# Kernel tuning notes

Measured on AMD Instinct MI355X. Metric: run time of the kernel, lower is better.

Reference implementation:

```python
import jax, jax.numpy as jnp
import numpy as np
from jax import lax

B, CIN, COUT, H, W, K = 8, 256, 256, 64, 64, 3
KK = K * K
PAD, STRIDE = 1, 1
EPS = 1e-5


def setup_inputs() -> dict:
    key = jax.random.key(0)
    k0, k1, k2 = jax.random.split(key, 3)
    x = jax.random.normal(k0, (B, CIN, H, W), jnp.float32)
    # offset/mask predicting conv: 3*K*K output channels (o1, o2, mask)
    w_off = jax.random.normal(k1, (3 * KK, CIN, K, K), jnp.float32) * 0.01
    b_off = jnp.zeros((3 * KK,), jnp.float32)
    # main deformable conv weight
    weight = jax.random.normal(k2, (COUT, CIN, K, K), jnp.float32) / np.sqrt(CIN * KK).astype(np.float32)
    bias = jnp.zeros((COUT,), jnp.float32)
    gamma = jnp.ones((COUT,), jnp.float32)
    beta = jnp.zeros((COUT,), jnp.float32)
    return {"x": x, "w_off": w_off, "b_off": b_off, "weight": weight,
            "bias": bias, "gamma": gamma, "beta": beta}


def _bilinear_sample(img, ph, pw):
    """img: [C,H,W]; ph,pw: [KK,H,W] float sample positions. Zero outside. -> [C,KK,H,W]"""
    h0 = jnp.floor(ph).astype(jnp.int32)
    w0 = jnp.floor(pw).astype(jnp.int32)
    h1, w1 = h0 + 1, w0 + 1
    lh = ph - h0.astype(ph.dtype)
    lw = pw - w0.astype(pw.dtype)
    hh, hw = 1.0 - lh, 1.0 - lw

    def corner(hi, wi):
        valid = (hi >= 0) & (hi < H) & (wi >= 0) & (wi < W)
        hc = jnp.clip(hi, 0, H - 1)
        wc = jnp.clip(wi, 0, W - 1)
        v = img[:, hc, wc]  # [C,KK,H,W]
        return v * valid.astype(img.dtype)[None]

    return (corner(h0, w0) * (hh * hw)[None] + corner(h0, w1) * (hh * lw)[None]
            + corner(h1, w0) * (lh * hw)[None] + corner(h1, w1) * (lh * lw)[None])


def _forward(x, w_off, b_off, weight, bias, gamma, beta):
    dn = ('NCHW', 'OIHW', 'NCHW')
    # offset/mask branch (standard conv)
    om = lax.conv_general_dilated(x, w_off, (STRIDE, STRIDE), ((PAD, PAD), (PAD, PAD)),
                                  dimension_numbers=dn) + b_off[None, :, None, None]
    o1, o2, m = jnp.split(om, 3, axis=1)
    offset = jnp.concatenate([o1, o2], axis=1)          # [B, 2*KK, H, W]
    off_h = offset[:, 0::2]                             # [B, KK, H, W] dy per tap
    off_w = offset[:, 1::2]                             # [B, KK, H, W] dx per tap
    mask = jax.nn.sigmoid(m)                            # [B, KK, H, W]

    taps = jnp.arange(KK)
    base_h = (taps // K - PAD).astype(jnp.float32)[:, None, None] \
        + (jnp.arange(H, dtype=jnp.float32) * STRIDE)[None, :, None]  # [KK,H,1]
    base_w = (taps % K - PAD).astype(jnp.float32)[:, None, None] \
        + (jnp.arange(W, dtype=jnp.float32) * STRIDE)[None, None, :]  # [KK,1,W]
    ph = base_h[None] + off_h                           # [B,KK,H,W]
    pw = base_w[None] + off_w

    sampled = jax.vmap(_bilinear_sample)(x, ph, pw)     # [B,CIN,KK,H,W]
    sampled = sampled * mask[:, None]                   # modulated (DCNv2)

    y = jnp.einsum('bckhw,ock->bohw', sampled, weight.reshape(COUT, CIN, KK))
    y = y + bias[None, :, None, None]

    # BatchNorm2d (training mode: batch statistics) + ReLU
    mean = y.mean(axis=(0, 2, 3))
    var = y.var(axis=(0, 2, 3))
    yn = (y - mean[None, :, None, None]) * lax.rsqrt(var + EPS)[None, :, None, None]
    out = jax.nn.relu(gamma[None, :, None, None] * yn + beta[None, :, None, None])
    return out


def reference(x, w_off, b_off, weight, bias, gamma, beta):
    return _forward(x, w_off, b_off, weight, bias, gamma, beta)
```

## Files before the change

kernel.cpp:

```cpp
#include <hip/hip_runtime.h>
#include <cstdint>

#define BB    8
#define CIN   256
#define COUT  256
#define HH    64
#define WW    64

typedef __attribute__((ext_vector_type(8))) short    s16x8;
typedef __attribute__((ext_vector_type(8))) unsigned short u16x8;
typedef __attribute__((ext_vector_type(4))) unsigned short u16x4;
typedef __attribute__((ext_vector_type(4))) float    f32x4;

__device__ __forceinline__ float bf2f(unsigned short u) {
    unsigned int v = ((unsigned int)u) << 16;
    return __builtin_bit_cast(float, v);
}
__device__ __forceinline__ unsigned short f2bf(float f) {
    unsigned int u = __builtin_bit_cast(unsigned int, f);
    unsigned int r = (u + 0x7FFFu + ((u >> 16) & 1u)) >> 16;
    return (unsigned short)r;
}

__global__ void k_pack(const float* __restrict__ x,
                       const float* __restrict__ w,
                       const float* __restrict__ woff,
                       unsigned short* __restrict__ xT,
                       unsigned short* __restrict__ wTk,
                       unsigned short* __restrict__ wofT) {
    int blk = blockIdx.x;
    int t = threadIdx.x;
    __shared__ float tile[64 * 65];
    if (blk < 2048) {
        int b    = blk & 7;
        int rest = blk >> 3;
        int h    = rest >> 2;
        int c0   = (rest & 3) * 64;
#pragma unroll
        for (int r = 0; r < 16; ++r) {
            int idx = t + r * 256;
            int i = idx >> 6, w_ = idx & 63;
            tile[i * 65 + w_] = x[(((b * 256 + c0 + i) * 64 + h) * 64) + w_];
        }
        __syncthreads();
#pragma unroll
        for (int r = 0; r < 2; ++r) {
            int idx = t + r * 256;
            int w_ = idx >> 3;
            int c8 = (idx & 7) * 8;
            u16x8 res;
#pragma unroll
            for (int k = 0; k < 8; ++k) res[k] = f2bf(tile[(c8 + k) * 65 + w_]);
            *reinterpret_cast<u16x8*>(&xT[((b * 64 + h) * 64 + w_) * 256 + c0 + c8]) = res;
        }
    } else if (blk < 4352) {
        int idx = (blk - 2048) * 256 + t;
        int j   = idx & 7;
        int q   = (idx >> 3) & 3;
        int o16 = (idx >> 5) & 15;
        int n16 = (idx >> 9) & 15;
        int kc  = (idx >> 13) & 7;
        int tp  = idx >> 16;
        int c = kc * 32 + q * 8 + j;
        int o = n16 * 16 + o16;
        wTk[idx] = f2bf(w[(o * 256 + c) * 9 + tp]);
    } else {
        int idx = (blk - 4352) * 256 + t;
        int c  = idx & 255;
        int j  = (idx >> 8) & 31;
        int tp = idx >> 13;
        wofT[idx] = f2bf((j < 27) ? woff[(j * 256 + c) * 9 + tp] : 0.f);
    }
}

__global__ __launch_bounds__(512, 4)
void k_main(const unsigned short* __restrict__ xT,
            const unsigned short* __restrict__ wTk,
            const unsigned short* __restrict__ wofT,
            const float* __restrict__ boffg,
            const float* __restrict__ bias,
            unsigned short* __restrict__ y16,
            float* __restrict__ gsum, float* __restrict__ gssq) {
    __shared__ __align__(16) char smem[76032];
    int blk = blockIdx.x;
    int b = blk & 7, h = blk >> 3;
    int pblk = b * 64 + h;
    int t = threadIdx.x;
    int lane = t & 63, wv = t >> 6;
    int lm = lane & 15, q = lane >> 4;
    const f32x4 FZ = {0.f, 0.f, 0.f, 0.f};

    {
        unsigned short* S3 = (unsigned short*)smem;
        float* OMS = (float*)(smem + 67584);
        f32x4 oacc0 = FZ, oacc1 = FZ;
        int p0w = wv * 16;
        for (int cc = 0; cc < 2; ++cc) {
            __syncthreads();
            if (t < 96) {
                int rr = t >> 5, col = (t >> 4) & 1, c8 = (t & 15) * 8;
                u16x8 z = {0,0,0,0,0,0,0,0};
                *reinterpret_cast<u16x8*>(&S3[(rr * 66 + col * 65) * 136 + c8]) = z;
            }
#pragma unroll
            for (int r = 0; r < 6; ++r) {
                int v = t + r * 512;
                int rr = v >> 10, rem = v & 1023;
                int w_ = rem >> 4, c8 = (rem & 15) * 8;
                int hr = h + rr - 1;
                u16x8 d = {0,0,0,0,0,0,0,0};
                if (hr >= 0 && hr < 64)
                    d = *reinterpret_cast<const u16x8*>(xT + ((b * 64 + hr) * 64 + w_) * 256 + cc * 128 + c8);
                *reinterpret_cast<u16x8*>(&S3[(rr * 66 + w_ + 1) * 136 + c8]) = d;
            }
            __syncthreads();
            if (wv < 4) {
#pragma unroll
                for (int tp = 0; tp < 9; ++tp) {
                    int dh = tp / 3, dw = tp % 3;
                    const unsigned short* wb = wofT + (tp * 32 + lm) * 256 + cc * 128;
#pragma unroll
                    for (int kc = 0; kc < 4; ++kc) {
                        s16x8 a = *reinterpret_cast<const s16x8*>(
                            &S3[(dh * 66 + p0w + lm + dw) * 136 + kc * 32 + q * 8]);
                        s16x8 b0 = *reinterpret_cast<const s16x8*>(wb + kc * 32 + q * 8);
                        s16x8 b1 = *reinterpret_cast<const s16x8*>(wb + 16 * 256 + kc * 32 + q * 8);
                        oacc0 = __builtin_amdgcn_mfma_f32_16x16x32_bf16(a, b0, oacc0, 0, 0, 0);
                        oacc1 = __builtin_amdgcn_mfma_f32_16x16x32_bf16(a, b1, oacc1, 0, 0, 0);
                    }
                }
            }
        }
        if (wv < 4) {
#pragma unroll
            for (int n = 0; n < 2; ++n) {
                int j = n * 16 + lm;
                float bj = (j < 27) ? boffg[j] : 0.f;
                f32x4 a = n ? oacc1 : oacc0;
#pragma unroll
                for (int i = 0; i < 4; ++i)
                    OMS[(p0w + q * 4 + i) * 33 + j] = a[i] + bj;
            }
        }
        __syncthreads();
    }

    unsigned short* S = (unsigned short*)smem;
    float* OMS = (float*)(smem + 67584);
    f32x4 acc[4][4];
#pragma unroll
    for (int m = 0; m < 4; ++m)
#pragma unroll
        for (int n = 0; n < 4; ++n) acc[m][n] = FZ;

    if (wv >= 4) {
        int pw = wv - 4;
        int s  = lane & 7;
        int pA = pw * 16 + (lane >> 3);
        int pB = pA + 8;
        int rb = b * 4096;

        float wgA[4], wgB[4];
        int   adA[4], adB[4];

        auto setup = [&](int tp, int p, float* wgt, int* ad) {
            float oh = OMS[p * 33 + 2 * tp];
            float ow = OMS[p * 33 + 2 * tp + 1];
            float mv = OMS[p * 33 + 18 + tp];
            float mk = 1.f / (1.f + __expf(-mv));
            float ph = (float)(h + tp / 3 - 1) + oh;
            float pw_ = (float)(p + tp % 3 - 1) + ow;
            float fh0 = floorf(ph), fw0 = floorf(pw_);
            int ih0 = (int)fh0, iw0 = (int)fw0;
            float lh = ph - fh0, lw = pw_ - fw0;
            float hh = 1.f - lh, hw_ = 1.f - lw;
            bool vh0 = (ih0 >= 0) & (ih0 < 64);
            bool vh1 = (ih0 + 1 >= 0) & (ih0 + 1 < 64);
            bool vw0 = (iw0 >= 0) & (iw0 < 64);
            bool vw1 = (iw0 + 1 >= 0) & (iw0 + 1 < 64);
            wgt[0] = hh * hw_ * mk * (float)(vh0 & vw0);
            wgt[1] = hh * lw  * mk * (float)(vh0 & vw1);
            wgt[2] = lh * hw_ * mk * (float)(vh1 & vw0);
            wgt[3] = lh * lw  * mk * (float)(vh1 & vw1);
            int ch0 = min(max(ih0, 0), 63), ch1 = min(max(ih0 + 1, 0), 63);
            int cw0 = min(max(iw0, 0), 63), cw1 = min(max(iw0 + 1, 0), 63);
            ad[0] = ((rb + ch0 * 64 + cw0) * 256);
            ad[1] = ((rb + ch0 * 64 + cw1) * 256);
            ad[2] = ((rb + ch1 * 64 + cw0) * 256);
            ad[3] = ((rb + ch1 * 64 + cw1) * 256);
        };

        u16x8 rP[4], rQ[4];
        auto issueSet = [&](const int* ad, int j, u16x8* r) {
            int off = j * 64 + s * 8;
#pragma unroll
            for (int c = 0; c < 4; ++c)
                r[c] = *reinterpret_cast<const u16x8*>(xT + ad[c] + off);
        };
        auto blendSet = [&](int buf, int p, const float* wgt, int j, u16x8* r) {
            u16x8 res;
#pragma unroll
            for (int k = 0; k < 8; ++k) {
                float v = wgt[0] * bf2f(r[0][k]);
                v = fmaf(wgt[1], bf2f(r[1][k]), v);
                v = fmaf(wgt[2], bf2f(r[2][k]), v);
                v = fmaf(wgt[3], bf2f(r[3][k]), v);
                res[k] = f2bf(v);
            }
            *reinterpret_cast<u16x8*>(&S[buf * 16896 + p * 264 + j * 64 + s * 8]) = res;
        };
        auto fillTap = [&](int tp, int buf) {
            setup(tp, pA, wgA, adA);
            setup(tp, pB, wgB, adB);
            issueSet(adA, 0, rP);
            issueSet(adA, 1, rQ);
            blendSet(buf, pA, wgA, 0, rP);  issueSet(adA, 2, rP);
            blendSet(buf, pA, wgA, 1, rQ);  issueSet(adA, 3, rQ);
            blendSet(buf, pA, wgA, 2, rP);  issueSet(adB, 0, rP);
            blendSet(buf, pA, wgA, 3, rQ);  issueSet(adB, 1, rQ);
            blendSet(buf, pB, wgB, 0, rP);  issueSet(adB, 2, rP);
            blendSet(buf, pB, wgB, 1, rQ);  issueSet(adB, 3, rQ);
            blendSet(buf, pB, wgB, 2, rP);
            blendSet(buf, pB, wgB, 3, rQ);
        };

        fillTap(0, 0);
        __syncthreads();
        for (int tp = 0; tp < 9; ++tp) {
            if (tp < 8) fillTap(tp + 1, (tp + 1) & 1);
            __syncthreads();
        }
    } else {
        __syncthreads();
        for (int tp = 0; tp < 9; ++tp) {
            const unsigned short* Sc = &S[(tp & 1) * 16896];
            const unsigned short* wtap = wTk + (size_t)tp * 65536
                                       + (size_t)(wv * 4) * 512 + lm * 32 + q * 8;
            s16x8 wbuf[2][4];
#pragma unroll
            for (int n = 0; n < 4; ++n)
                wbuf[0][n] = *reinterpret_cast<const s16x8*>(wtap + n * 512);
#pragma unroll
            for (int kc = 0; kc < 8; ++kc) {
                if (kc < 7) {
                    const unsigned short* wb = wtap + (kc + 1) * 8192;
#pragma unroll
                    for (int n = 0; n < 4; ++n)
                        wbuf[(kc + 1) & 1][n] = *reinterpret_cast<const s16x8*>(wb + n * 512);
                }
#pragma unroll
                for (int mt = 0; mt < 4; ++mt) {
                    s16x8 a = *reinterpret_cast<const s16x8*>(
                        &Sc[(mt * 16 + lm) * 264 + kc * 32 + q * 8]);
#pragma unroll
                    for (int n = 0; n < 4; ++n)
                        acc[mt][n] = __builtin_amdgcn_mfma_f32_16x16x32_bf16(
                            a, wbuf[kc & 1][n], acc[mt][n], 0, 0, 0);
                }
            }
            __syncthreads();
        }
    }

    if (wv < 4) {
        u16x4* yv = reinterpret_cast<u16x4*>(y16);
#pragma unroll
        for (int nt = 0; nt < 4; ++nt) {
            int o = wv * 64 + nt * 16 + lm;
            float bo = bias[o];
            float sacc = 0.f, ssacc = 0.f;
#pragma unroll
            for (int mt = 0; mt < 4; ++mt) {
                u16x4 st;
#pragma unroll
                for (int i = 0; i < 4; ++i) {
                    float v = acc[mt][nt][i] + bo;
                    st[i] = f2bf(v);
                    sacc += v; ssacc += v * v;
                }
                int idx4 = ((pblk * 4 + wv) * 16 + nt * 4 + mt) * 64 + lane;
                yv[idx4] = st;
            }
            sacc  += __shfl_xor(sacc, 16);
            sacc  += __shfl_xor(sacc, 32);
            ssacc += __shfl_xor(ssacc, 16);
            ssacc += __shfl_xor(ssacc, 32);
            if (q == 0) {
                atomicAdd(&gsum[o], sacc);
                atomicAdd(&gssq[o], ssacc);
            }
        }
    }
}

__global__ void k_bnrelu(const unsigned short* __restrict__ y16,
                         const float* __restrict__ gsum, const float* __restrict__ gssq,
                         const float* __restrict__ gamma, const float* __restrict__ beta,
                         float* __restrict__ out) {
    int blk = blockIdx.x;
    int b = blk & 7, h = blk >> 3;
    int pblk = b * 64 + h;
    __shared__ unsigned short T[64 * 257];
    __shared__ float sc[256], sh[256];
    int t = threadIdx.x;
    {
        const float n = 32768.f;
        float mean = gsum[t] / n;
        float var = gssq[t] / n - mean * mean;
        float inv = rsqrtf(var + 1e-5f);
        float s = gamma[t] * inv;
        sc[t] = s;
        sh[t] = beta[t] - mean * s;
    }
    const u16x4* yv = reinterpret_cast<const u16x4*>(y16) + pblk * 4096;
#pragma unroll
    for (int r = 0; r < 16; ++r) {
        int v = t + r * 256;
        u16x4 d = yv[v];
        int lane = v & 63, mt = (v >> 6) & 3, nt = (v >> 8) & 3, wvv = (v >> 10) & 3;
        int p = mt * 16 + (lane >> 4) * 4;
        int o = wvv * 64 + nt * 16 + (lane & 15);
        T[(p + 0) * 257 + o] = d[0];
        T[(p + 1) * 257 + o] = d[1];
        T[(p + 2) * 257 + o] = d[2];
        T[(p + 3) * 257 + o] = d[3];
    }
    __syncthreads();
    int w4   = (t & 15) * 4;
    int orow = t >> 4;
    float* obase = out + (size_t)b * (256 * 4096) + h * 64;
#pragma unroll
    for (int it = 0; it < 16; ++it) {
        int o = orow + it * 16;
        float scl = sc[o], shf = sh[o];
        float4 vo;
        vo.x = fmaxf(bf2f(T[(w4 + 0) * 257 + o]) * scl + shf, 0.f);
        vo.y = fmaxf(bf2f(T[(w4 + 1) * 257 + o]) * scl + shf, 0.f);
        vo.z = fmaxf(bf2f(T[(w4 + 2) * 257 + o]) * scl + shf, 0.f);
        vo.w = fmaxf(bf2f(T[(w4 + 3) * 257 + o]) * scl + shf, 0.f);
        *reinterpret_cast<float4*>(obase + (size_t)o * 4096 + w4) = vo;
    }
}

extern "C" void kernel_launch(void* const* d_in, const int* in_sizes, int n_in,
                              void* d_out, int out_size, void* d_ws, size_t ws_size,
                              hipStream_t stream) {
    const float* x      = (const float*)d_in[0];
    const float* w_off  = (const float*)d_in[1];
    const float* b_off  = (const float*)d_in[2];
    const float* weight = (const float*)d_in[3];
    const float* bias   = (const float*)d_in[4];
    const float* gamma  = (const float*)d_in[5];
    const float* beta   = (const float*)d_in[6];

    char* ws = (char*)d_ws;
    const size_t OFF_XT    = 0;
    const size_t OFF_WT    = OFF_XT + 16777216;
    const size_t OFF_WOFT  = OFF_WT + 1179648;
    const size_t OFF_Y16   = OFF_WOFT + 147456;
    const size_t OFF_SUM   = OFF_Y16 + 16777216;
    const size_t OFF_SUMSQ = OFF_SUM + 1024;

    unsigned short* xT   = (unsigned short*)(ws + OFF_XT);
    unsigned short* wTk  = (unsigned short*)(ws + OFF_WT);
    unsigned short* wofT = (unsigned short*)(ws + OFF_WOFT);
    unsigned short* y16  = (unsigned short*)(ws + OFF_Y16);
    float* gsum  = (float*)(ws + OFF_SUM);
    float* gssq  = (float*)(ws + OFF_SUMSQ);

    hipMemsetAsync(ws + OFF_SUM, 0, 2048, stream);

    k_pack  <<<4640, 256, 0, stream>>>(x, weight, w_off, xT, wTk, wofT);
    k_main  <<< 512, 512, 0, stream>>>(xT, wTk, wofT, b_off, bias, y16, gsum, gssq);
    k_bnrelu<<< 512, 256, 0, stream>>>(y16, gsum, gssq, gamma, beta, (float*)d_out);
}
```

Before: 207.2 us.

## Split offset conv across all waves, prefetch weights, fold memset, truncate bf16

The offset/mask conv prologue now uses all 8 waves instead of 4. Each group of 4 waves takes one half of the channel chunk, and the two partial sums are combined through a shared-memory buffer. Per-tap weight fragments are prefetched one tap ahead, the stats memset moves into the pack kernel, and the blend rounding switches from round-to-nearest to truncation. The aim is to shorten the serial prologue where half the block sat idle and to cut launch and ALU overhead, at the cost of an extra reduction pass with its barriers and slightly lower bf16 accuracy.

```diff
diff --git a/kernel.cpp b/kernel.cpp
--- a/kernel.cpp
+++ b/kernel.cpp
@@ -21,16 +21,22 @@
     unsigned int r = (u + 0x7FFFu + ((u >> 16) & 1u)) >> 16;
     return (unsigned short)r;
 }
+__device__ __forceinline__ unsigned short f2bf_rz(float f) {
+    return (unsigned short)(__builtin_bit_cast(unsigned int, f) >> 16);
+}
 
 __global__ void k_pack(const float* __restrict__ x,
                        const float* __restrict__ w,
                        const float* __restrict__ woff,
                        unsigned short* __restrict__ xT,
                        unsigned short* __restrict__ wTk,
-                       unsigned short* __restrict__ wofT) {
+                       unsigned short* __restrict__ wofT,
+                       float* __restrict__ gsum,
+                       float* __restrict__ gssq) {
     int blk = blockIdx.x;
     int t = threadIdx.x;
     __shared__ float tile[64 * 65];
+    if (blk == 0 && t < 256) { gsum[t] = 0.f; gssq[t] = 0.f; }
     if (blk < 2048) {
         int b    = blk & 7;
         int rest = blk >> 3;
@@ -92,9 +98,12 @@
 
     {
         unsigned short* S3 = (unsigned short*)smem;
-        float* OMS = (float*)(smem + 67584);
+        float* PART = (float*)(smem + 53856);
+        float* OMS  = (float*)(smem + 67584);
         f32x4 oacc0 = FZ, oacc1 = FZ;
-        int p0w = wv * 16;
+        int myTile = wv & 3;
+        int myKH   = wv >> 2;
+        int p0w = myTile * 16;
         for (int cc = 0; cc < 2; ++cc) {
             __syncthreads();
             if (t < 96) {
@@ -114,23 +123,48 @@
                 *reinterpret_cast<u16x8*>(&S3[(rr * 66 + w_ + 1) * 136 + c8]) = d;
             }
             __syncthreads();
-            if (wv < 4) {
+            {
+                int boff = cc * 128 + myKH * 64 + q * 8;
+                s16x8 pb[4], nb[4];
+                {
+                    const unsigned short* wb = wofT + (0 * 32 + lm) * 256 + boff;
+                    pb[0] = *reinterpret_cast<const s16x8*>(wb);
+                    pb[1] = *reinterpret_cast<const s16x8*>(wb + 32);
+                    pb[2] = *reinterpret_cast<const s16x8*>(wb + 16 * 256);
+                    pb[3] = *reinterpret_cast<const s16x8*>(wb + 16 * 256 + 32);
+                }
 #pragma unroll
                 for (int tp = 0; tp < 9; ++tp) {
-                    int dh = tp / 3, dw = tp % 3;
-                    const unsigned short* wb = wofT + (tp * 32 + lm) * 256 + cc * 128;
-#pragma unroll
-                    for (int kc = 0; kc < 4; ++kc) {
-                        s16x8 a = *reinterpret_cast<const s16x8*>(
-                            &S3[(dh * 66 + p0w + lm + dw) * 136 + kc * 32 + q * 8]);
-                        s16x8 b0 = *reinterpret_cast<const s16x8*>(wb + kc * 32 + q * 8);
-                        s16x8 b1 = *reinterpret_cast<const s16x8*>(wb + 16 * 256 + kc * 32 + q * 8);
-                        oacc0 = __builtin_amdgcn_mfma_f32_16x16x32_bf16(a, b0, oacc0, 0, 0, 0);
-                        oacc1 = __builtin_amdgcn_mfma_f32_16x16x32_bf16(a, b1, oacc1, 0, 0, 0);
+                    if (tp < 8) {
+                        const unsigned short* wb = wofT + ((tp + 1) * 32 + lm) * 256 + boff;
+                        nb[0] = *reinterpret_cast<const s16x8*>(wb);
+                        nb[1] = *reinterpret_cast<const s16x8*>(wb + 32);
+                        nb[2] = *reinterpret_cast<const s16x8*>(wb + 16 * 256);
+                        nb[3] = *reinterpret_cast<const s16x8*>(wb + 16 * 256 + 32);
                     }
-                }
-            }
-        }
+                    int dh = tp / 3, dw_ = tp % 3;
+                    int arow = (dh * 66 + p0w + lm + dw_) * 136 + myKH * 64 + q * 8;
+                    s16x8 a0 = *reinterpret_cast<const s16x8*>(&S3[arow]);
+                    s16x8 a1 = *reinterpret_cast<const s16x8*>(&S3[arow + 32]);
+                    oacc0 = __builtin_amdgcn_mfma_f32_16x16x32_bf16(a0, pb[0], oacc0, 0, 0, 0);
+                    oacc0 = __builtin_amdgcn_mfma_f32_16x16x32_bf16(a1, pb[1], oacc0, 0, 0, 0);
+                    oacc1 = __builtin_amdgcn_mfma_f32_16x16x32_bf16(a0, pb[2], oacc1, 0, 0, 0);
+                    oacc1 = __builtin_amdgcn_mfma_f32_16x16x32_bf16(a1, pb[3], oacc1, 0, 0, 0);
+#pragma unroll
+                    for (int i = 0; i < 4; ++i) pb[i] = nb[i];
+                }
+            }
+        }
+        __syncthreads();
+        if (wv >= 4) {
+#pragma unroll
+            for (int i = 0; i < 4; ++i) {
+                int prow = p0w + q * 4 + i;
+                PART[prow * 33 + lm]      = oacc0[i];
+                PART[prow * 33 + 16 + lm] = oacc1[i];
+            }
+        }
+        __syncthreads();
         if (wv < 4) {
 #pragma unroll
             for (int n = 0; n < 2; ++n) {
@@ -138,8 +172,10 @@
                 float bj = (j < 27) ? boffg[j] : 0.f;
                 f32x4 a = n ? oacc1 : oacc0;
 #pragma unroll
-                for (int i = 0; i < 4; ++i)
-                    OMS[(p0w + q * 4 + i) * 33 + j] = a[i] + bj;
+                for (int i = 0; i < 4; ++i) {
+                    int prow = p0w + q * 4 + i;
+                    OMS[prow * 33 + j] = a[i] + PART[prow * 33 + j] + bj;
+                }
             }
         }
         __syncthreads();
@@ -205,7 +241,7 @@
                 v = fmaf(wgt[1], bf2f(r[1][k]), v);
                 v = fmaf(wgt[2], bf2f(r[2][k]), v);
                 v = fmaf(wgt[3], bf2f(r[3][k]), v);
-                res[k] = f2bf(v);
+                res[k] = f2bf_rz(v);
             }
             *reinterpret_cast<u16x8*>(&S[buf * 16896 + p * 264 + j * 64 + s * 8]) = res;
         };
@@ -368,9 +404,7 @@
     float* gsum  = (float*)(ws + OFF_SUM);
     float* gssq  = (float*)(ws + OFF_SUMSQ);
 
-    hipMemsetAsync(ws + OFF_SUM, 0, 2048, stream);
-
-    k_pack  <<<4640, 256, 0, stream>>>(x, weight, w_off, xT, wTk, wofT);
+    k_pack  <<<4640, 256, 0, stream>>>(x, weight, w_off, xT, wTk, wofT, gsum, gssq);
     k_main  <<< 512, 512, 0, stream>>>(xT, wTk, wofT, b_off, bias, y16, gsum, gssq);
     k_bnrelu<<< 512, 256, 0, stream>>>(y16, gsum, gssq, gamma, beta, (float*)d_out);
 }
```

After: 200.9 us. 1.03x faster.
